# Optimization experiments

Measured on AMD Instinct MI355X. Metric: run time of the kernel, lower is better.

## Reference

```python
import jax, jax.numpy as jnp
import numpy as np

N_Q = 10000
B, S = 128, 200
M = 50          # memory_size
DK = 64         # memory_key_state_dim == q_embed_dim == final_fc_dim
DV = 128        # memory_value_state_dim == qa_embed_dim
F = 64          # final_fc_dim


def setup_inputs() -> dict:
    key = jax.random.key(0)
    ks = jax.random.split(key, 14)
    q_data = jax.random.randint(ks[0], (B, S), 0, N_Q + 1)
    qa_data = jax.random.randint(ks[1], (B, S), 0, 2 * N_Q + 1)
    # target in {-1 (pad), 0, 1}
    target = jax.random.randint(ks[2], (B, S), -1, 2).astype(jnp.float32)
    q_embed_w = jax.random.normal(ks[3], (N_Q + 1, DK), jnp.float32) * 0.1
    q_embed_w = q_embed_w.at[0].set(0.0)  # padding_idx=0
    qa_embed_w = jax.random.normal(ks[4], (2 * N_Q + 1, DV), jnp.float32) * 0.1
    qa_embed_w = qa_embed_w.at[0].set(0.0)
    mem_key = jax.random.normal(ks[5], (M, DK), jnp.float32) * (2.0 / DK) ** 0.5
    init_mem_value = jax.random.normal(ks[6], (M, DV), jnp.float32) * (2.0 / DV) ** 0.5
    erase_w = jax.random.normal(ks[7], (DV, DV), jnp.float32) * (2.0 / DV) ** 0.5
    erase_b = jnp.zeros((DV,), jnp.float32)
    add_w = jax.random.normal(ks[8], (DV, DV), jnp.float32) * (2.0 / DV) ** 0.5
    add_b = jnp.zeros((DV,), jnp.float32)
    read_w = jax.random.normal(ks[9], (F, DV + F), jnp.float32) * (2.0 / (DV + F)) ** 0.5
    read_b = jnp.zeros((F,), jnp.float32)
    pred_w = jax.random.normal(ks[10], (1, F), jnp.float32) * (2.0 / F) ** 0.5
    pred_b = jnp.zeros((1,), jnp.float32)
    return {
        'q_data': q_data, 'qa_data': qa_data, 'target': target,
        'q_embed_w': q_embed_w, 'qa_embed_w': qa_embed_w,
        'mem_key': mem_key, 'init_mem_value': init_mem_value,
        'erase_w': erase_w, 'erase_b': erase_b,
        'add_w': add_w, 'add_b': add_b,
        'read_w': read_w, 'read_b': read_b,
        'pred_w': pred_w, 'pred_b': pred_b,
    }


def reference(q_data, qa_data, target, q_embed_w, qa_embed_w, mem_key,
              init_mem_value, erase_w, erase_b, add_w, add_b,
              read_w, read_b, pred_w, pred_b):
    q_e = q_embed_w[q_data]    # [B,S,DK]
    qa_e = qa_embed_w[qa_data]  # [B,S,DV]
    Mv0 = jnp.broadcast_to(init_mem_value, (q_data.shape[0],) + init_mem_value.shape)  # [B,M,DV]

    def step(Mv, x):
        q, qa = x                                           # [B,DK], [B,DV]
        w = jax.nn.softmax(q @ mem_key.T, axis=1)           # addressing -> [B,M]
        read = jnp.einsum('bm,bmv->bv', w, Mv)              # weighted read (before write)
        e = jax.nn.sigmoid(qa @ erase_w.T + erase_b)        # [B,DV]
        a = jnp.tanh(qa @ add_w.T + add_b)                  # [B,DV]
        Mv_new = Mv * (1.0 - w[:, :, None] * e[:, None, :]) + w[:, :, None] * a[:, None, :]
        return Mv_new, read

    _, reads = jax.lax.scan(step, Mv0, (q_e.transpose(1, 0, 2), qa_e.transpose(1, 0, 2)))
    reads = reads.transpose(1, 0, 2)                        # [B,S,DV]

    h = jnp.tanh(jnp.concatenate([reads, q_e], axis=-1) @ read_w.T + read_b)  # [B,S,F]
    logits = (h @ pred_w.T + pred_b)[..., 0]                # [B,S]

    mask = target >= 0
    t = jnp.where(mask, target, 0.0)
    # stable BCE with logits
    bce = jnp.maximum(logits, 0.0) - logits * t + jnp.log1p(jnp.exp(-jnp.abs(logits)))
    n_valid = jnp.maximum(jnp.sum(mask.astype(jnp.float32)), 1.0)
    loss = jnp.sum(jnp.where(mask, bce, 0.0)) / n_valid
    probs = jnp.where(mask, jax.nn.sigmoid(logits), 0.0)    # masked predictions, fixed shape
    return loss, probs
```

## Files before the change

### kernel.cpp

```cpp
#include <hip/hip_runtime.h>
#include <math.h>

#define BB 128
#define SS 200
#define MM 50
#define DKK 64
#define DVV 128
#define FF 64
#define NROW (BB*SS)

#define WROW 64
#define NFCB (NROW/64)
#define WLDS 136
#define FLDS 200
#define CLEN 25
#define MP 25
#define NSCB 100

#define W_OFF   0L
#define EA_OFF  (W_OFF + (long)NROW*WROW)
#define R_OFF   (EA_OFF + (long)NROW*DVV*2)
#define ACC_OFF (R_OFF + (long)NROW*DVV)

typedef __attribute__((ext_vector_type(8))) short bf16x8;
typedef __attribute__((ext_vector_type(4))) float f32x4;
typedef __attribute__((ext_vector_type(2))) float f32x2;

__device__ __forceinline__ float rlane(float v, int l) {
    return __builtin_bit_cast(float, __builtin_amdgcn_readlane(__builtin_bit_cast(unsigned, v), l));
}
__device__ __forceinline__ short f2bf(float f) {
    unsigned u = __builtin_bit_cast(unsigned, f);
    u += 0x7fff + ((u >> 16) & 1);
    return (short)(u >> 16);
}
__device__ __forceinline__ bf16x8 cvt8(const float* p) {
    float4 lo = *(const float4*)p;
    float4 hi = *(const float4*)(p + 4);
    bf16x8 f;
    f[0] = f2bf(lo.x); f[1] = f2bf(lo.y); f[2] = f2bf(lo.z); f[3] = f2bf(lo.w);
    f[4] = f2bf(hi.x); f[5] = f2bf(hi.y); f[6] = f2bf(hi.z); f[7] = f2bf(hi.w);
    return f;
}

__global__ __launch_bounds__(256) void k_pre(const int* __restrict__ q_data,
                                             const float* __restrict__ q_embed_w,
                                             const float* __restrict__ mem_key,
                                             const int* __restrict__ qa_data,
                                             const float* __restrict__ qa_embed_w,
                                             const float* __restrict__ erase_w,
                                             const float* __restrict__ erase_b,
                                             const float* __restrict__ add_w,
                                             const float* __restrict__ add_b,
                                             float* __restrict__ w_out,
                                             float* __restrict__ EA,
                                             float* __restrict__ acc) {
    __shared__ union {
        short  wl[2 * 128 * WLDS];
        float4 mk[MM * 16];
    } sh;
    int tid = threadIdx.x;
    int bid = blockIdx.x;

    if (bid < NSCB) {
        if (bid == 0 && tid == 0) {
            acc[0] = 0.f; acc[1] = 0.f;
            ((unsigned*)acc)[2] = 0u;
        }
        const float4* mkg = (const float4*)mem_key;
        for (int i = tid; i < MM * 16; i += 256) sh.mk[i] = mkg[i];
        __syncthreads();

        int item = bid * 256 + tid;
        int qidx = q_data[item];
        const float4* qg = (const float4*)(q_embed_w + (long)qidx * DKK);
        float4 q[16];
#pragma unroll
        for (int i = 0; i < 16; i++) q[i] = qg[i];

        float s[MM];
        float mx = -1e30f;
#pragma unroll 2
        for (int m = 0; m < MM; m++) {
            float a = 0.f;
#pragma unroll
            for (int k4 = 0; k4 < 16; k4++) {
                float4 mkv = sh.mk[m * 16 + k4];
                float4 qv = q[k4];
                a = fmaf(qv.x, mkv.x, a);
                a = fmaf(qv.y, mkv.y, a);
                a = fmaf(qv.z, mkv.z, a);
                a = fmaf(qv.w, mkv.w, a);
            }
            s[m] = a;
            mx = fmaxf(mx, a);
        }
        float sum = 0.f;
#pragma unroll
        for (int m = 0; m < MM; m++) { s[m] = expf(s[m] - mx); sum += s[m]; }
        float inv = 1.f / sum;

        float* wo = w_out + (long)item * WROW;
#pragma unroll
        for (int m = 0; m < MM; m++) wo[m] = s[m] * inv;
#pragma unroll
        for (int m = MM; m < WROW; m++) wo[m] = 0.f;
        return;
    }

    int r0 = (bid - NSCB) * 64;
    int lane = tid & 63;
    int wv = tid >> 6;
    int n = lane & 15;
    int quad = lane >> 4;

    for (int i = tid; i < 8192; i += 256) {
        int mat = i >> 12;
        int r = (i >> 5) & 127;
        int p = i & 31;
        float4 src = *(const float4*)((mat ? add_w : erase_w) + r * 128 + p * 4);
        short4 d;
        d.x = f2bf(src.x); d.y = f2bf(src.y); d.z = f2bf(src.z); d.w = f2bf(src.w);
        *(short4*)(sh.wl + (mat * 128 + r) * WLDS + p * 4) = d;
    }

    int arow = r0 + wv * 16 + n;
    int qidx = qa_data[arow];
    const float* qp = qa_embed_w + (long)qidx * DVV + quad * 8;
    bf16x8 afrag[4];
#pragma unroll
    for (int kb = 0; kb < 4; kb++) afrag[kb] = cvt8(qp + kb * 32);

    float eb_[8], ab_[8];
#pragma unroll
    for (int vt = 0; vt < 8; vt++) {
        eb_[vt] = erase_b[vt * 16 + n];
        ab_[vt] = add_b[vt * 16 + n];
    }
    __syncthreads();

    int rowbase = r0 + wv * 16 + quad * 4;
#pragma unroll 2
    for (int vt = 0; vt < 8; vt++) {
        int vrow = vt * 16 + n;
        f32x4 ae = {0.f, 0.f, 0.f, 0.f};
        f32x4 aa = {0.f, 0.f, 0.f, 0.f};
#pragma unroll
        for (int kb = 0; kb < 4; kb++) {
            bf16x8 be = *(const bf16x8*)(sh.wl + vrow * WLDS + kb * 32 + quad * 8);
            bf16x8 ba = *(const bf16x8*)(sh.wl + (128 + vrow) * WLDS + kb * 32 + quad * 8);
            ae = __builtin_amdgcn_mfma_f32_16x16x32_bf16(afrag[kb], be, ae, 0, 0, 0);
            aa = __builtin_amdgcn_mfma_f32_16x16x32_bf16(afrag[kb], ba, aa, 0, 0, 0);
        }
        int v = vt * 16 + n;
        float eb = eb_[vt], ab = ab_[vt];
#pragma unroll
        for (int r = 0; r < 4; r++) {
            float ev = 1.f / (1.f + __expf(-(ae[r] + eb)));
            float av = 2.f / (1.f + __expf(-2.f * (aa[r] + ab))) - 1.f;
            float2 o; o.x = ev; o.y = av;
            *(float2*)(EA + (((long)(rowbase + r)) * DVV + v) * 2) = o;
        }
    }
}

__global__ __launch_bounds__(512, 2) void k_scan(const float* __restrict__ w_pad,
                                                 const float* __restrict__ EA,
                                                 const float* __restrict__ init_mv,
                                                 float* __restrict__ R) {
    __shared__ float Sb[MM * 64];
    int b   = blockIdx.x >> 1;
    int vh  = blockIdx.x & 1;
    int tid = threadIdx.x;
    int lane  = tid & 63;
    int chunk = tid >> 6;
    int v  = vh * 64 + lane;
    int t0 = chunk * CLEN;

    const float* wbase = w_pad + ((long)b * SS + t0) * WROW;
    const float* eab   = EA + (((long)b * SS + t0) * DVV + v) * 2;
    float*       Rb    = R + ((long)b * SS + t0) * DVV + v;

    const f32x2 one = {1.f, 1.f};

    f32x2 A2[MP], B2[MP];
#pragma unroll
    for (int j = 0; j < MP; j++) { A2[j] = one; B2[j] = (f32x2){0.f, 0.f}; }

    float  w_cur  = wbase[lane];
    float2 ea_cur = *(const float2*)eab;
#pragma unroll 1
    for (int t = 0; t < CLEN; t++) {
        int tp = (t + 1 < CLEN) ? t + 1 : t;
        float  w_nxt  = wbase[tp * WROW + lane];
        float2 ea_nxt = *(const float2*)(eab + (long)tp * DVV * 2);
        f32x2 e2 = {ea_cur.x, ea_cur.x};
        f32x2 a2 = {ea_cur.y, ea_cur.y};
#pragma unroll
        for (int j = 0; j < MP; j++) {
            f32x2 w2 = {rlane(w_cur, 2 * j), rlane(w_cur, 2 * j + 1)};
            f32x2 alpha = one - w2 * e2;
            A2[j] = A2[j] * alpha;
            B2[j] = alpha * B2[j] + w2 * a2;
        }
        w_cur = w_nxt; ea_cur = ea_nxt;
    }

    f32x2 Mv[MP];
    if (chunk == 0) {
#pragma unroll
        for (int j = 0; j < MP; j++) {
            Mv[j].x = init_mv[(2 * j) * DVV + v];
            Mv[j].y = init_mv[(2 * j + 1) * DVV + v];
        }
#pragma unroll
        for (int j = 0; j < MP; j++) {
            f32x2 nb = A2[j] * Mv[j] + B2[j];
            Sb[(2 * j) * 64 + lane] = nb.x;
            Sb[(2 * j + 1) * 64 + lane] = nb.y;
        }
    }
    __syncthreads();
    for (int c = 1; c < 8; c++) {
        if (chunk == c) {
#pragma unroll
            for (int j = 0; j < MP; j++) {
                Mv[j].x = Sb[(2 * j) * 64 + lane];
                Mv[j].y = Sb[(2 * j + 1) * 64 + lane];
            }
            if (c < 7) {
#pragma unroll
                for (int j = 0; j < MP; j++) {
                    f32x2 nb = A2[j] * Mv[j] + B2[j];
                    Sb[(2 * j) * 64 + lane] = nb.x;
                    Sb[(2 * j + 1) * 64 + lane] = nb.y;
                }
            }
        }
        __syncthreads();
    }

    w_cur  = wbase[lane];
    ea_cur = *(const float2*)eab;
#pragma unroll 1
    for (int t = 0; t < CLEN; t++) {
        int tp = (t + 1 < CLEN) ? t + 1 : t;
        float  w_nxt  = wbase[tp * WROW + lane];
        float2 ea_nxt = *(const float2*)(eab + (long)tp * DVV * 2);
        f32x2 e2 = {ea_cur.x, ea_cur.x};
        f32x2 a2 = {ea_cur.y, ea_cur.y};
        f32x2 rd2 = {0.f, 0.f};
#pragma unroll
        for (int j = 0; j < MP; j++) {
            f32x2 w2 = {rlane(w_cur, 2 * j), rlane(w_cur, 2 * j + 1)};
            rd2 = rd2 + w2 * Mv[j];
            f32x2 alpha = one - w2 * e2;
            Mv[j] = alpha * Mv[j] + w2 * a2;
        }
        Rb[t * DVV] = rd2.x + rd2.y;
        w_cur = w_nxt; ea_cur = ea_nxt;
    }
}

__global__ __launch_bounds__(256) void k_fc(const float* __restrict__ Rr,
                                            const int* __restrict__ q_data,
                                            const float* __restrict__ q_embed_w,
                                            const float* __restrict__ read_w,
                                            const float* __restrict__ read_b,
                                            const float* __restrict__ pred_w,
                                            const float* __restrict__ pred_b,
                                            const float* __restrict__ target,
                                            float* __restrict__ out,
                                            float* __restrict__ acc) {
    __shared__ short Wl[64 * FLDS];
    __shared__ float2 red[4];
    int tid = threadIdx.x;
    int r0 = blockIdx.x * 64;
    int lane = tid & 63;
    int wv = tid >> 6;
    int n = lane & 15;
    int quad = lane >> 4;

    for (int i = tid; i < 3072; i += 256) {
        int f = i / 48, p = i - f * 48;
        float4 src = *(const float4*)(read_w + f * 192 + p * 4);
        short4 d;
        d.x = f2bf(src.x); d.y = f2bf(src.y); d.z = f2bf(src.z); d.w = f2bf(src.w);
        *(short4*)(Wl + f * FLDS + p * 4) = d;
    }

    int arow = r0 + wv * 16 + n;
    const float* rp = Rr + (long)arow * DVV + quad * 8;
    int qi = q_data[arow];
    const float* qp = q_embed_w + (long)qi * DKK + quad * 8;
    bf16x8 afrag[6];
#pragma unroll
    for (int kb = 0; kb < 4; kb++) afrag[kb] = cvt8(rp + kb * 32);
#pragma unroll
    for (int kb = 0; kb < 2; kb++) afrag[4 + kb] = cvt8(qp + kb * 32);

    float rb_[4], pw_[4];
#pragma unroll
    for (int ft = 0; ft < 4; ft++) {
        rb_[ft] = read_b[ft * 16 + n];
        pw_[ft] = pred_w[ft * 16 + n];
    }
    float pb = pred_b[0];
    __syncthreads();

    int rowbase = r0 + wv * 16 + quad * 4;
    float pv[4] = {0.f, 0.f, 0.f, 0.f};
#pragma unroll
    for (int ft = 0; ft < 4; ft++) {
        int f = ft * 16 + n;
        f32x4 ac = {0.f, 0.f, 0.f, 0.f};
#pragma unroll
        for (int kb = 0; kb < 6; kb++) {
            bf16x8 bfr = *(const bf16x8*)(Wl + f * FLDS + kb * 32 + quad * 8);
            ac = __builtin_amdgcn_mfma_f32_16x16x32_bf16(afrag[kb], bfr, ac, 0, 0, 0);
        }
        float rb = rb_[ft], pw = pw_[ft];
#pragma unroll
        for (int r = 0; r < 4; r++) {
            float h = 2.f / (1.f + __expf(-2.f * (ac[r] + rb))) - 1.f;
            pv[r] = fmaf(pw, h, pv[r]);
        }
    }

    float bce_sum = 0.f, cnt = 0.f;
#pragma unroll
    for (int r = 0; r < 4; r++) {
        float p = pv[r];
        p += __shfl_xor(p, 1, 64);
        p += __shfl_xor(p, 2, 64);
        p += __shfl_xor(p, 4, 64);
        p += __shfl_xor(p, 8, 64);
        if (n == 0) {
            int row = rowbase + r;
            float tgt = target[row];
            float logit = p + pb;
            float prob = 0.f;
            if (tgt >= 0.f) {
                prob = 1.f / (1.f + __expf(-logit));
                float bce = fmaxf(logit, 0.f) - logit * tgt + log1pf(__expf(-fabsf(logit)));
                bce_sum += bce;
                cnt += 1.f;
            }
            out[1 + row] = prob;
        }
    }
    bce_sum += __shfl_xor(bce_sum, 16, 64);
    bce_sum += __shfl_xor(bce_sum, 32, 64);
    cnt     += __shfl_xor(cnt, 16, 64);
    cnt     += __shfl_xor(cnt, 32, 64);
    if (lane == 0) { red[wv].x = bce_sum; red[wv].y = cnt; }
    __syncthreads();
    if (tid == 0) {
        float bsum = red[0].x + red[1].x + red[2].x + red[3].x;
        float csum = red[0].y + red[1].y + red[2].y + red[3].y;
        atomicAdd(&acc[0], bsum);
        atomicAdd(&acc[1], csum);
        __threadfence();
        unsigned prev = atomicAdd((unsigned*)acc + 2, 1u);
        if (prev == NFCB - 1) {
            __threadfence();
            float B = atomicAdd(&acc[0], 0.f);
            float C = atomicAdd(&acc[1], 0.f);
            out[0] = B / fmaxf(C, 1.f);
        }
    }
}

extern "C" void kernel_launch(void* const* d_in, const int* in_sizes, int n_in,
                              void* d_out, int out_size, void* d_ws, size_t ws_size,
                              hipStream_t stream) {
    const int*   q_data     = (const int*)d_in[0];
    const int*   qa_data    = (const int*)d_in[1];
    const float* target     = (const float*)d_in[2];
    const float* q_embed_w  = (const float*)d_in[3];
    const float* qa_embed_w = (const float*)d_in[4];
    const float* mem_key    = (const float*)d_in[5];
    const float* init_mv    = (const float*)d_in[6];
    const float* erase_w    = (const float*)d_in[7];
    const float* erase_b    = (const float*)d_in[8];
    const float* add_w      = (const float*)d_in[9];
    const float* add_b      = (const float*)d_in[10];
    const float* read_w     = (const float*)d_in[11];
    const float* read_b     = (const float*)d_in[12];
    const float* pred_w     = (const float*)d_in[13];
    const float* pred_b     = (const float*)d_in[14];
    float* out = (float*)d_out;
    float* ws  = (float*)d_ws;

    float* w_all = ws + W_OFF;
    float* EA    = ws + EA_OFF;
    float* R     = ws + R_OFF;
    float* acc   = ws + ACC_OFF;

    k_pre<<<NSCB + NROW / 64, 256, 0, stream>>>(q_data, q_embed_w, mem_key,
                                                qa_data, qa_embed_w,
                                                erase_w, erase_b, add_w, add_b,
                                                w_all, EA, acc);
    k_scan<<<BB * 2, 512, 0, stream>>>(w_all, EA, init_mv, R);
    k_fc<<<NFCB, 256, 0, stream>>>(R, q_data, q_embed_w, read_w, read_b,
                                   pred_w, pred_b, target, out, acc);
}
```

Baseline: 182.5 us.

## Split scan memory slots across two waves and batch erase/add GEMM rows

The scan kernel now uses 1024 threads per block: each time chunk gets two waves, and each wave handles half of the 50 memory slots. Partial reads are combined through shared memory at the end. This halves the serial per-step work per wave, at the cost of fewer registers per thread and extra LDS traffic and sync. Separately, each erase/add projection block now processes 256 rows instead of 64, which amortizes the per-block conversion of the weights to bf16 in LDS.

```diff
diff --git a/kernel.cpp b/kernel.cpp
--- a/kernel.cpp
+++ b/kernel.cpp
@@ -14,8 +14,9 @@
 #define WLDS 136
 #define FLDS 200
 #define CLEN 25
-#define MP 25
+#define MH 25
 #define NSCB 100
+#define NEAB 100
 
 #define W_OFF   0L
 #define EA_OFF  (W_OFF + (long)NROW*WROW)
@@ -24,7 +25,6 @@
 
 typedef __attribute__((ext_vector_type(8))) short bf16x8;
 typedef __attribute__((ext_vector_type(4))) float f32x4;
-typedef __attribute__((ext_vector_type(2))) float f32x2;
 
 __device__ __forceinline__ float rlane(float v, int l) {
     return __builtin_bit_cast(float, __builtin_amdgcn_readlane(__builtin_bit_cast(unsigned, v), l));
@@ -108,7 +108,7 @@
         return;
     }
 
-    int r0 = (bid - NSCB) * 64;
+    int r0 = (bid - NSCB) * 256;
     int lane = tid & 63;
     int wv = tid >> 6;
     int n = lane & 15;
@@ -124,12 +124,15 @@
         *(short4*)(sh.wl + (mat * 128 + r) * WLDS + p * 4) = d;
     }
 
-    int arow = r0 + wv * 16 + n;
-    int qidx = qa_data[arow];
-    const float* qp = qa_embed_w + (long)qidx * DVV + quad * 8;
-    bf16x8 afrag[4];
-#pragma unroll
-    for (int kb = 0; kb < 4; kb++) afrag[kb] = cvt8(qp + kb * 32);
+    bf16x8 afrag[4][4];
+#pragma unroll
+    for (int rt = 0; rt < 4; rt++) {
+        int arow = r0 + rt * 64 + wv * 16 + n;
+        int qidx = qa_data[arow];
+        const float* qp = qa_embed_w + (long)qidx * DVV + quad * 8;
+#pragma unroll
+        for (int kb = 0; kb < 4; kb++) afrag[rt][kb] = cvt8(qp + kb * 32);
+    }
 
     float eb_[8], ab_[8];
 #pragma unroll
@@ -139,53 +142,65 @@
     }
     __syncthreads();
 
-    int rowbase = r0 + wv * 16 + quad * 4;
-#pragma unroll 2
+#pragma unroll 1
     for (int vt = 0; vt < 8; vt++) {
         int vrow = vt * 16 + n;
-        f32x4 ae = {0.f, 0.f, 0.f, 0.f};
-        f32x4 aa = {0.f, 0.f, 0.f, 0.f};
+        f32x4 ae[4], aa[4];
+#pragma unroll
+        for (int rt = 0; rt < 4; rt++) {
+            ae[rt] = (f32x4){0.f, 0.f, 0.f, 0.f};
+            aa[rt] = (f32x4){0.f, 0.f, 0.f, 0.f};
+        }
 #pragma unroll
         for (int kb = 0; kb < 4; kb++) {
             bf16x8 be = *(const bf16x8*)(sh.wl + vrow * WLDS + kb * 32 + quad * 8);
             bf16x8 ba = *(const bf16x8*)(sh.wl + (128 + vrow) * WLDS + kb * 32 + quad * 8);
-            ae = __builtin_amdgcn_mfma_f32_16x16x32_bf16(afrag[kb], be, ae, 0, 0, 0);
-            aa = __builtin_amdgcn_mfma_f32_16x16x32_bf16(afrag[kb], ba, aa, 0, 0, 0);
+#pragma unroll
+            for (int rt = 0; rt < 4; rt++) {
+                ae[rt] = __builtin_amdgcn_mfma_f32_16x16x32_bf16(afrag[rt][kb], be, ae[rt], 0, 0, 0);
+                aa[rt] = __builtin_amdgcn_mfma_f32_16x16x32_bf16(afrag[rt][kb], ba, aa[rt], 0, 0, 0);
+            }
         }
         int v = vt * 16 + n;
         float eb = eb_[vt], ab = ab_[vt];
 #pragma unroll
-        for (int r = 0; r < 4; r++) {
-            float ev = 1.f / (1.f + __expf(-(ae[r] + eb)));
-            float av = 2.f / (1.f + __expf(-2.f * (aa[r] + ab))) - 1.f;
-            float2 o; o.x = ev; o.y = av;
-            *(float2*)(EA + (((long)(rowbase + r)) * DVV + v) * 2) = o;
-        }
-    }
-}
-
-__global__ __launch_bounds__(512, 2) void k_scan(const float* __restrict__ w_pad,
-                                                 const float* __restrict__ EA,
-                                                 const float* __restrict__ init_mv,
-                                                 float* __restrict__ R) {
+        for (int rt = 0; rt < 4; rt++) {
+            int rowbase = r0 + rt * 64 + wv * 16 + quad * 4;
+#pragma unroll
+            for (int r = 0; r < 4; r++) {
+                float ev = 1.f / (1.f + __expf(-(ae[rt][r] + eb)));
+                float av = 2.f / (1.f + __expf(-2.f * (aa[rt][r] + ab))) - 1.f;
+                float2 o; o.x = ev; o.y = av;
+                *(float2*)(EA + (((long)(rowbase + r)) * DVV + v) * 2) = o;
+            }
+        }
+    }
+}
+
+__global__ __launch_bounds__(1024, 1) void k_scan(const float* __restrict__ w_pad,
+                                                  const float* __restrict__ EA,
+                                                  const float* __restrict__ init_mv,
+                                                  float* __restrict__ R) {
     __shared__ float Sb[MM * 64];
+    __shared__ float Rp[8 * CLEN * 64];
     int b   = blockIdx.x >> 1;
     int vh  = blockIdx.x & 1;
     int tid = threadIdx.x;
-    int lane  = tid & 63;
-    int chunk = tid >> 6;
+    int lane = tid & 63;
+    int wave = tid >> 6;
+    int tc = wave >> 1;
+    int mh = wave & 1;
     int v  = vh * 64 + lane;
-    int t0 = chunk * CLEN;
+    int t0 = tc * CLEN;
+    int mbase = mh * MH;
 
     const float* wbase = w_pad + ((long)b * SS + t0) * WROW;
     const float* eab   = EA + (((long)b * SS + t0) * DVV + v) * 2;
     float*       Rb    = R + ((long)b * SS + t0) * DVV + v;
 
-    const f32x2 one = {1.f, 1.f};
-
-    f32x2 A2[MP], B2[MP];
-#pragma unroll
-    for (int j = 0; j < MP; j++) { A2[j] = one; B2[j] = (f32x2){0.f, 0.f}; }
+    float A[MH], Bc[MH];
+#pragma unroll
+    for (int j = 0; j < MH; j++) { A[j] = 1.f; Bc[j] = 0.f; }
 
     float  w_cur  = wbase[lane];
     float2 ea_cur = *(const float2*)eab;
@@ -194,47 +209,32 @@
         int tp = (t + 1 < CLEN) ? t + 1 : t;
         float  w_nxt  = wbase[tp * WROW + lane];
         float2 ea_nxt = *(const float2*)(eab + (long)tp * DVV * 2);
-        f32x2 e2 = {ea_cur.x, ea_cur.x};
-        f32x2 a2 = {ea_cur.y, ea_cur.y};
-#pragma unroll
-        for (int j = 0; j < MP; j++) {
-            f32x2 w2 = {rlane(w_cur, 2 * j), rlane(w_cur, 2 * j + 1)};
-            f32x2 alpha = one - w2 * e2;
-            A2[j] = A2[j] * alpha;
-            B2[j] = alpha * B2[j] + w2 * a2;
+        float e = ea_cur.x, a = ea_cur.y;
+#pragma unroll
+        for (int j = 0; j < MH; j++) {
+            float wm = rlane(w_cur, mbase + j);
+            float alpha = fmaf(-wm, e, 1.f);
+            A[j] *= alpha;
+            Bc[j] = fmaf(alpha, Bc[j], wm * a);
         }
         w_cur = w_nxt; ea_cur = ea_nxt;
     }
 
-    f32x2 Mv[MP];
-    if (chunk == 0) {
-#pragma unroll
-        for (int j = 0; j < MP; j++) {
-            Mv[j].x = init_mv[(2 * j) * DVV + v];
-            Mv[j].y = init_mv[(2 * j + 1) * DVV + v];
-        }
-#pragma unroll
-        for (int j = 0; j < MP; j++) {
-            f32x2 nb = A2[j] * Mv[j] + B2[j];
-            Sb[(2 * j) * 64 + lane] = nb.x;
-            Sb[(2 * j + 1) * 64 + lane] = nb.y;
-        }
+    float Mv[MH];
+    if (tc == 0) {
+#pragma unroll
+        for (int j = 0; j < MH; j++) Mv[j] = init_mv[(mbase + j) * DVV + v];
+#pragma unroll
+        for (int j = 0; j < MH; j++) Sb[(mbase + j) * 64 + lane] = fmaf(A[j], Mv[j], Bc[j]);
     }
     __syncthreads();
     for (int c = 1; c < 8; c++) {
-        if (chunk == c) {
-#pragma unroll
-            for (int j = 0; j < MP; j++) {
-                Mv[j].x = Sb[(2 * j) * 64 + lane];
-                Mv[j].y = Sb[(2 * j + 1) * 64 + lane];
-            }
+        if (tc == c) {
+#pragma unroll
+            for (int j = 0; j < MH; j++) Mv[j] = Sb[(mbase + j) * 64 + lane];
             if (c < 7) {
 #pragma unroll
-                for (int j = 0; j < MP; j++) {
-                    f32x2 nb = A2[j] * Mv[j] + B2[j];
-                    Sb[(2 * j) * 64 + lane] = nb.x;
-                    Sb[(2 * j + 1) * 64 + lane] = nb.y;
-                }
+                for (int j = 0; j < MH; j++) Sb[(mbase + j) * 64 + lane] = fmaf(A[j], Mv[j], Bc[j]);
             }
         }
         __syncthreads();
@@ -242,23 +242,30 @@
 
     w_cur  = wbase[lane];
     ea_cur = *(const float2*)eab;
+    float rdbuf[CLEN];
 #pragma unroll 1
     for (int t = 0; t < CLEN; t++) {
         int tp = (t + 1 < CLEN) ? t + 1 : t;
         float  w_nxt  = wbase[tp * WROW + lane];
         float2 ea_nxt = *(const float2*)(eab + (long)tp * DVV * 2);
-        f32x2 e2 = {ea_cur.x, ea_cur.x};
-        f32x2 a2 = {ea_cur.y, ea_cur.y};
-        f32x2 rd2 = {0.f, 0.f};
-#pragma unroll
-        for (int j = 0; j < MP; j++) {
-            f32x2 w2 = {rlane(w_cur, 2 * j), rlane(w_cur, 2 * j + 1)};
-            rd2 = rd2 + w2 * Mv[j];
-            f32x2 alpha = one - w2 * e2;
-            Mv[j] = alpha * Mv[j] + w2 * a2;
-        }
-        Rb[t * DVV] = rd2.x + rd2.y;
+        float e = ea_cur.x, a = ea_cur.y;
+        float rd = 0.f;
+#pragma unroll
+        for (int j = 0; j < MH; j++) {
+            float wm = rlane(w_cur, mbase + j);
+            rd = fmaf(wm, Mv[j], rd);
+            float alpha = fmaf(-wm, e, 1.f);
+            Mv[j] = fmaf(alpha, Mv[j], wm * a);
+        }
+        if (mh == 0) Rp[(tc * CLEN + t) * 64 + lane] = rd;
+        else         rdbuf[t] = rd;
         w_cur = w_nxt; ea_cur = ea_nxt;
+    }
+    __syncthreads();
+    if (mh == 1) {
+#pragma unroll
+        for (int t = 0; t < CLEN; t++)
+            Rb[t * DVV] = rdbuf[t] + Rp[(tc * CLEN + t) * 64 + lane];
     }
 }
 
@@ -397,11 +404,11 @@
     float* R     = ws + R_OFF;
     float* acc   = ws + ACC_OFF;
 
-    k_pre<<<NSCB + NROW / 64, 256, 0, stream>>>(q_data, q_embed_w, mem_key,
-                                                qa_data, qa_embed_w,
-                                                erase_w, erase_b, add_w, add_b,
-                                                w_all, EA, acc);
-    k_scan<<<BB * 2, 512, 0, stream>>>(w_all, EA, init_mv, R);
+    k_pre<<<NSCB + NEAB, 256, 0, stream>>>(q_data, q_embed_w, mem_key,
+                                           qa_data, qa_embed_w,
+                                           erase_w, erase_b, add_w, add_b,
+                                           w_all, EA, acc);
+    k_scan<<<BB * 2, 1024, 0, stream>>>(w_all, EA, init_mv, R);
     k_fc<<<NFCB, 256, 0, stream>>>(R, q_data, q_embed_w, read_w, read_b,
                                    pred_w, pred_b, target, out, acc);
 }
```

Measured after the change: 226.8 us. +24.3%, slower.
